# Performance work log

Hardware: AMD Instinct MI355X
Metric: run time of the kernel (lower is better)

## Reference

```python
import jax, jax.numpy as jnp
import numpy as np

N, E, B, D, OUT_D = 10000, 160000, 64, 1024, 128

def setup_inputs() -> dict:
    key = jax.random.key(0)
    ks = jax.random.split(key, 18)
    s = 0.02
    return {
        "pro1_x": jax.random.normal(ks[0], (N, D), jnp.float32),
        "pro1_edge_index": jax.random.randint(ks[1], (2, E), 0, N, jnp.int64 if jax.config.jax_enable_x64 else jnp.int32),
        "pro1_batch": jnp.sort(jax.random.randint(ks[2], (N,), 0, B)),
        "pro2_x": jax.random.normal(ks[3], (N, D), jnp.float32),
        "pro2_edge_index": jax.random.randint(ks[4], (2, E), 0, N, jnp.int64 if jax.config.jax_enable_x64 else jnp.int32),
        "pro2_batch": jnp.sort(jax.random.randint(ks[5], (N,), 0, B)),
        "W1": jax.random.normal(ks[6], (D, D), jnp.float32) * s,
        "b1": jnp.zeros((D,), jnp.float32),
        "fc1_W": jax.random.normal(ks[7], (D, OUT_D), jnp.float32) * s,
        "fc1_b": jnp.zeros((OUT_D,), jnp.float32),
        "W2": jax.random.normal(ks[8], (D, D), jnp.float32) * s,
        "b2": jnp.zeros((D,), jnp.float32),
        "fc2_W": jax.random.normal(ks[9], (D, OUT_D), jnp.float32) * s,
        "fc2_b": jnp.zeros((OUT_D,), jnp.float32),
        "final_W": jax.random.normal(ks[10], (2 * OUT_D, 1), jnp.float32) * s,
        "final_b": jnp.zeros((1,), jnp.float32),
    }

def leaky_relu(x):
    return jnp.where(x >= 0, x, 0.01 * x)

def gcn_conv(x, edge_index, W, b):
    # PyG GCNConv with default add_self_loops + symmetric normalization
    src, dst = edge_index[0], edge_index[1]
    h = x @ W  # [N, D]
    deg = jnp.zeros((x.shape[0],), x.dtype).at[dst].add(1.0) + 1.0  # in-degree + self-loop
    dinv = jax.lax.rsqrt(deg)
    norm = dinv[src] * dinv[dst]  # [E]
    agg = jax.ops.segment_sum(h[src] * norm[:, None], dst, num_segments=x.shape[0])
    agg = agg + h * (1.0 / deg)[:, None]  # self-loop contribution: deg^-1/2 * deg^-1/2
    return agg + b

def global_mean_pool(x, batch, num_graphs):
    sums = jax.ops.segment_sum(x, batch, num_segments=num_graphs)
    cnt = jax.ops.segment_sum(jnp.ones((x.shape[0],), x.dtype), batch, num_segments=num_graphs)
    return sums / jnp.maximum(cnt, 1.0)[:, None]

def reference(pro1_x, pro1_edge_index, pro1_batch, pro2_x, pro2_edge_index, pro2_batch,
              W1, b1, fc1_W, fc1_b, W2, b2, fc2_W, fc2_b, final_W, final_b):
    # branch 1
    x = leaky_relu(gcn_conv(pro1_x, pro1_edge_index, W1, b1))
    x = global_mean_pool(x, pro1_batch, B)
    x = leaky_relu(x @ fc1_W + fc1_b)  # dropout is identity in eval
    # branch 2
    xt = leaky_relu(gcn_conv(pro2_x, pro2_edge_index, W2, b2))
    xt = global_mean_pool(xt, pro2_batch, B)
    xt = leaky_relu(xt @ fc2_W + fc2_b)
    combined = jnp.concatenate([x, xt], axis=1)  # [B, 256]
    return combined @ final_W + final_b
```

## Files before the change

### kernel.cpp

```cpp
#include <hip/hip_runtime.h>
#include <stdint.h>

typedef __attribute__((ext_vector_type(8))) short short8;
typedef __attribute__((ext_vector_type(8))) __bf16 bf16x8;
typedef __attribute__((ext_vector_type(4))) float f32x4;

__device__ inline unsigned short f2bf(float f) {
  unsigned u = __float_as_uint(f);
  unsigned r = (u + 0x7FFFu + ((u >> 16) & 1u)) >> 16;
  return (unsigned short)r;
}
__device__ inline float bflo(unsigned v) { return __uint_as_float(v << 16); }
__device__ inline float bfhi(unsigned v) { return __uint_as_float(v & 0xFFFF0000u); }
__device__ inline bf16x8 as_bf(short8 v) { return __builtin_bit_cast(bf16x8, v); }

#define GLOAD_LDS16(gp, lp)                                                   \
  __builtin_amdgcn_global_load_lds(                                           \
      (const __attribute__((address_space(1))) void*)(gp),                    \
      (__attribute__((address_space(3))) void*)(lp), 16, 0, 0)

#define NG 2048
#define NSL 8

__global__ void prep1_kernel(const float* __restrict__ x0, const float* __restrict__ x1,
                             unsigned short* __restrict__ xb0, unsigned short* __restrict__ xb1,
                             const float* __restrict__ W0, const float* __restrict__ W1,
                             unsigned short* __restrict__ Wt0, unsigned short* __restrict__ Wt1,
                             const int* __restrict__ ei0, const int* __restrict__ ei1,
                             int* __restrict__ dg0, int* __restrict__ dg1,
                             int n, int mpad, int E, int CB) {
  __shared__ float tile[32][33];
  int br = blockIdx.y;
  int b = blockIdx.x;
  int t = threadIdx.x;
  if (b < CB) {
    const float* x = br ? x1 : x0;
    unsigned short* xb = br ? xb1 : xb0;
    long i = (long)b * 256 + t;
    long total = (long)mpad * 128;
    if (i >= total) return;
    long e0 = i * 8;
    int row = (int)(e0 >> 10);
    short8 v;
    if (row < n) {
      const float* s = x + e0;
      float4 fa = *(const float4*)(s);
      float4 fb = *(const float4*)(s + 4);
      v[0] = (short)f2bf(fa.x); v[1] = (short)f2bf(fa.y);
      v[2] = (short)f2bf(fa.z); v[3] = (short)f2bf(fa.w);
      v[4] = (short)f2bf(fb.x); v[5] = (short)f2bf(fb.y);
      v[6] = (short)f2bf(fb.z); v[7] = (short)f2bf(fb.w);
    } else {
      v = (short8)0;
    }
    *(short8*)(xb + e0) = v;
  } else if (b < CB + 1024) {
    const float* W = br ? W1 : W0;
    unsigned short* Wt = br ? Wt1 : Wt0;
    int bb = b - CB;
    int bx = bb & 31;
    int by = bb >> 5;
    int tx = t & 31, ty = t >> 5;
#pragma unroll
    for (int r = 0; r < 4; ++r) {
      int k = by * 32 + ty + r * 8;
      tile[ty + r * 8][tx] = W[(long)k * 1024 + bx * 32 + tx];
    }
    __syncthreads();
#pragma unroll
    for (int r = 0; r < 4; ++r) {
      int nrow = bx * 32 + ty + r * 8;
      int kcol = by * 32 + tx;
      Wt[(long)nrow * 1024 + kcol] = f2bf(tile[tx][ty + r * 8]);
    }
  } else {
    const int* ei = br ? ei1 : ei0;
    int* degi = br ? dg1 : dg0;
    int e = (b - CB - 1024) * 256 + t;
    if (e >= E) return;
    atomicAdd(&degi[ei[E + e]], 1);
  }
}

__global__ __launch_bounds__(1024) void scan2_kernel(
    const int* __restrict__ degA, int* __restrict__ offA, int* __restrict__ curA,
    const int* __restrict__ degB, int* __restrict__ offB, int* __restrict__ curB, int n) {
  const int* deg = blockIdx.x ? degB : degA;
  int* off = blockIdx.x ? offB : offA;
  int* cur = blockIdx.x ? curB : curA;
  __shared__ int wsum[17];
  int t = threadIdx.x, lane = t & 63, w = t >> 6;
  int CH = (n + 1023) >> 10;
  int i0 = t * CH;
  int s = 0;
  for (int i = 0; i < CH; ++i) {
    int idx = i0 + i;
    s += (idx < n) ? ((deg[idx] + 4) & ~3) : 0;
  }
  int inc = s;
  for (int d = 1; d < 64; d <<= 1) {
    int x = __shfl_up(inc, d);
    if (lane >= d) inc += x;
  }
  if (lane == 63) wsum[w] = inc;
  __syncthreads();
  if (t == 0) {
    int r = 0;
    for (int k = 0; k < 16; ++k) { int x = wsum[k]; wsum[k] = r; r += x; }
    wsum[16] = r;
  }
  __syncthreads();
  int run = wsum[w] + inc - s;
  for (int i = 0; i < CH; ++i) {
    int idx = i0 + i;
    if (idx < n) {
      off[idx] = run;
      cur[idx] = run;
      run += (deg[idx] + 4) & ~3;
    }
  }
  if (t == 0) off[n] = wsum[16];
}

__global__ void prep2_kernel(const int* __restrict__ ei0, const int* __restrict__ ei1,
                             const int* __restrict__ dg0, const int* __restrict__ dg1,
                             int* __restrict__ cur0, int* __restrict__ cur1,
                             uint2* __restrict__ cw0, uint2* __restrict__ cw1,
                             const int* __restrict__ off0, const int* __restrict__ off1,
                             int* __restrict__ rng0, int* __restrict__ rng1,
                             int E, int N, int FB) {
  int br = blockIdx.y;
  int b = blockIdx.x;
  int t = threadIdx.x;
  if (b < FB) {
    const int* ei = br ? ei1 : ei0;
    const int* dg = br ? dg1 : dg0;
    int* cur = br ? cur1 : cur0;
    uint2* cw = br ? cw1 : cw0;
    int e = b * 256 + t;
    if (e >= E + N) return;
    int s, d; float w;
    if (e < E) {
      s = ei[e]; d = ei[E + e];
      w = rsqrtf((float)(dg[s] + 1)) * rsqrtf((float)(dg[d] + 1));
    } else {
      s = e - E; d = s;
      w = 1.0f / (float)(dg[s] + 1);
    }
    int p = atomicAdd(&cur[d], 1);
    uint2 v; v.x = (unsigned)s * 2048u; v.y = __float_as_uint(w);
    cw[p] = v;
  } else {
    const int* off = br ? off1 : off0;
    int* rng = br ? rng1 : rng0;
    int q = (b - FB) * 256 + t;
    if (q > NG) return;
    if (q == NG) { rng[q] = N; return; }
    long Etot = off[N];
    long target = (long)q * Etot;
    int lo = 0, hi = N;
    while (lo < hi) {
      int mid = (lo + hi) >> 1;
      if ((long)off[mid] * NG >= target) hi = mid; else lo = mid + 1;
    }
    rng[q] = lo;
  }
}

#define BM 128
#define BN 128
#define BK 64

__global__ __launch_bounds__(256) void gemm_bf16_kernel(
    const unsigned short* __restrict__ A0, const unsigned short* __restrict__ A1,
    const unsigned short* __restrict__ B0, const unsigned short* __restrict__ B1,
    unsigned short* __restrict__ C0, unsigned short* __restrict__ C1,
    int Nn, int K) {
  const unsigned short* A = blockIdx.z ? A1 : A0;
  const unsigned short* Bt = blockIdx.z ? B1 : B0;
  unsigned short* C = blockIdx.z ? C1 : C0;
  __shared__ alignas(16) unsigned short As[BM * BK];
  __shared__ alignas(16) unsigned short Bs[BN * BK];
  int x = blockIdx.x;
  long m0 = (long)((x >> 6) * 8 + (x & 7)) * BM;
  long n0 = (long)((x >> 3) & 7) * BN;
  int t = threadIdx.x;
  int lane = t & 63;
  int w = t >> 6;
  int wm = (w >> 1) * 64, wn = (w & 1) * 64;
  int l3 = lane >> 3;
  int gsw = (lane & 7) ^ l3;
  int srowb = w * 8 + l3;
  const unsigned short* Ag = A + (m0 + srowb) * K + gsw * 8;
  const unsigned short* Bg = Bt + (n0 + srowb) * K + gsw * 8;
  unsigned short* AsP = As + t * 8;
  unsigned short* BsP = Bs + t * 8;
  int fr = lane & 15;
  int c0 = (lane >> 4) ^ (lane & 7);
  const unsigned short* afp0 = As + (wm + fr) * BK + c0 * 8;
  const unsigned short* afp1 = As + (wm + fr) * BK + (c0 ^ 4) * 8;
  const unsigned short* bfp0 = Bs + (wn + fr) * BK + c0 * 8;
  const unsigned short* bfp1 = Bs + (wn + fr) * BK + (c0 ^ 4) * 8;
  f32x4 acc[4][4] = {};
  for (int k0 = 0; k0 < K; k0 += BK) {
    __syncthreads();
#pragma unroll
    for (int j = 0; j < 4; ++j) {
      GLOAD_LDS16(Ag + (long)(j * 32) * K + k0, AsP + j * 2048);
      GLOAD_LDS16(Bg + (long)(j * 32) * K + k0, BsP + j * 2048);
    }
    __syncthreads();
    short8 af[4][2], bf[4][2];
#pragma unroll
    for (int i = 0; i < 4; ++i) {
      af[i][0] = *(const short8*)(afp0 + i * 16 * BK);
      af[i][1] = *(const short8*)(afp1 + i * 16 * BK);
    }
#pragma unroll
    for (int i = 0; i < 4; ++i) {
      bf[i][0] = *(const short8*)(bfp0 + i * 16 * BK);
      bf[i][1] = *(const short8*)(bfp1 + i * 16 * BK);
    }
#pragma unroll
    for (int i = 0; i < 4; ++i)
#pragma unroll
      for (int j = 0; j < 4; ++j) {
        acc[i][j] = __builtin_amdgcn_mfma_f32_16x16x32_bf16(as_bf(af[i][0]), as_bf(bf[j][0]),
                                                            acc[i][j], 0, 0, 0);
        acc[i][j] = __builtin_amdgcn_mfma_f32_16x16x32_bf16(as_bf(af[i][1]), as_bf(bf[j][1]),
                                                            acc[i][j], 0, 0, 0);
      }
  }
  int cr = (lane >> 4) * 4;
  int cc = lane & 15;
#pragma unroll
  for (int i = 0; i < 4; ++i)
#pragma unroll
    for (int j = 0; j < 4; ++j) {
      long row = m0 + wm + i * 16 + cr;
      long col = n0 + wn + j * 16 + cc;
      unsigned short* cp = C + row * Nn + col;
#pragma unroll
      for (int r = 0; r < 4; ++r)
        cp[(long)r * Nn] = f2bf(acc[i][j][r]);
    }
}

__global__ __launch_bounds__(256) void agg_pool_kernel(
    const unsigned short* __restrict__ H0, const unsigned short* __restrict__ H1,
    const int* __restrict__ off0, const int* __restrict__ off1,
    const uint2* __restrict__ cw0, const uint2* __restrict__ cw1,
    const int* __restrict__ b0, const int* __restrict__ b1,
    const int* __restrict__ rng0, const int* __restrict__ rng1,
    const float* __restrict__ bias0, const float* __restrict__ bias1,
    float* __restrict__ pool0, float* __restrict__ pool1,
    float* __restrict__ scr0, float* __restrict__ scr1,
    int* __restrict__ gid0, int* __restrict__ gid1) {
  int br = blockIdx.y;
  const uint8_t* Hb = (const uint8_t*)(br ? H1 : H0);
  const int* off = br ? off1 : off0;
  const uint2* cw = br ? cw1 : cw0;
  const int* batch = br ? b1 : b0;
  const int* rng = br ? rng1 : rng0;
  const float* bias = br ? bias1 : bias0;
  float* pool = br ? pool1 : pool0;
  float* scratch = br ? scr1 : scr0;
  int* gid = br ? gid1 : gid0;

  int t = threadIdx.x;
  int wv = t >> 6, lane = t & 63, qw = lane >> 4, l16 = lane & 15;
  int slice = blockIdx.x & 7;
  int part = blockIdx.x >> 3;
  int q = part * 4 + wv;
  int d0 = slice * 128 + l16 * 8;
  unsigned d0b = (unsigned)d0 * 2;
  int na = rng[q], nb = rng[q + 1];
  int g0 = -1, g1 = -1;
  if (na < nb) {
    float4 bv0 = *(const float4*)(bias + d0);
    float4 bv1 = *(const float4*)(bias + d0 + 4);
    float bv[8] = {bv0.x, bv0.y, bv0.z, bv0.w, bv1.x, bv1.y, bv1.z, bv1.w};
    float pacc[8] = {};
    float a[8] = {};
    int curg = batch[na];
    int fi = 0;
    int nd = na;
    int ee = off[na + 1];
    int eend = off[nb];
    int e = off[na];
    uint2 cc = cw[e + qw];
    uint2 cn = cw[e + 4 + qw];
    uint4 hc = *(const uint4*)(Hb + (cc.x + d0b));
#pragma unroll 2
    for (; e < eend; e += 4) {
      uint4 hn = *(const uint4*)(Hb + (cn.x + d0b));
      uint2 c2 = cw[e + 8 + qw];
      float w = __uint_as_float(cc.y);
      a[0] += w * bflo(hc.x); a[1] += w * bfhi(hc.x);
      a[2] += w * bflo(hc.y); a[3] += w * bfhi(hc.y);
      a[4] += w * bflo(hc.z); a[5] += w * bfhi(hc.z);
      a[6] += w * bflo(hc.w); a[7] += w * bfhi(hc.w);
      cc = cn; cn = c2; hc = hn;
      if (e + 4 == ee) {
#pragma unroll
        for (int k = 0; k < 8; ++k) {
          float v = a[k];
          v += __shfl_xor(v, 16);
          v += __shfl_xor(v, 32);
          v += bv[k];
          pacc[k] += (v >= 0.f) ? v : 0.01f * v;
          a[k] = 0.f;
        }
        ++nd;
        if (nd < nb) {
          ee = off[nd + 1];
          int g = batch[nd];
          if (g != curg) {
            if (fi == 0) {
              g0 = curg;
              if (qw == 0) {
                float* sp = scratch + ((long)q * 2 + 0) * 1024 + d0;
                *(float4*)sp = make_float4(pacc[0], pacc[1], pacc[2], pacc[3]);
                *(float4*)(sp + 4) = make_float4(pacc[4], pacc[5], pacc[6], pacc[7]);
              }
            } else {
              if (qw == 0) {
                float* pp = pool + (long)curg * 1024 + d0;
#pragma unroll
                for (int k = 0; k < 8; ++k) atomicAdd(pp + k, pacc[k]);
              }
            }
            ++fi;
#pragma unroll
            for (int k = 0; k < 8; ++k) pacc[k] = 0.f;
            curg = g;
          }
        }
      }
    }
    if (fi == 0) {
      g0 = curg;
      if (qw == 0) {
        float* sp = scratch + ((long)q * 2 + 0) * 1024 + d0;
        *(float4*)sp = make_float4(pacc[0], pacc[1], pacc[2], pacc[3]);
        *(float4*)(sp + 4) = make_float4(pacc[4], pacc[5], pacc[6], pacc[7]);
      }
    } else {
      g1 = curg;
      if (qw == 0) {
        float* sp = scratch + ((long)q * 2 + 1) * 1024 + d0;
        *(float4*)sp = make_float4(pacc[0], pacc[1], pacc[2], pacc[3]);
        *(float4*)(sp + 4) = make_float4(pacc[4], pacc[5], pacc[6], pacc[7]);
      }
    }
  }
  if (slice == 0 && lane == 0) {
    gid[q * 2] = g0;
    gid[q * 2 + 1] = g1;
  }
}

__global__ __launch_bounds__(256) void pool_reduce_kernel(
    const float* __restrict__ scr0, const float* __restrict__ scr1,
    const int* __restrict__ gid0, const int* __restrict__ gid1,
    const int* __restrict__ b0, const int* __restrict__ b1,
    const int* __restrict__ rng0, const int* __restrict__ rng1,
    float* __restrict__ pool0, float* __restrict__ pool1, int N) {
  int br = blockIdx.y;
  const float* scratch = br ? scr1 : scr0;
  const int* gid = br ? gid1 : gid0;
  const int* batch = br ? b1 : b0;
  const int* rng = br ? rng1 : rng0;
  float* pool = br ? pool1 : pool0;
  int g = blockIdx.x >> 2;
  int slice = blockIdx.x & 3;
  int tid = threadIdx.x;
  int lo = 0, hi = N;
  while (lo < hi) { int m = (lo + hi) >> 1; if (batch[m] < g) lo = m + 1; else hi = m; }
  int gs = lo;
  lo = 0; hi = N;
  while (lo < hi) { int m = (lo + hi) >> 1; if (batch[m] <= g) lo = m + 1; else hi = m; }
  int ge = lo;
  if (gs >= ge) return;
  lo = 0; hi = NG - 1;
  while (lo < hi) { int m = (lo + hi) >> 1; if (rng[m + 1] > gs) hi = m; else lo = m + 1; }
  int qlo = lo;
  lo = 0; hi = NG - 1;
  while (lo < hi) { int m = (lo + hi + 1) >> 1; if (rng[m] < ge) lo = m; else hi = m - 1; }
  int qhi = lo;
  float s = 0.f;
  for (int q = qlo; q <= qhi; ++q) {
    int a = gid[q * 2], b = gid[q * 2 + 1];
    if (a == g) s += scratch[((long)q * 2 + 0) * 1024 + slice * 256 + tid];
    if (b == g) s += scratch[((long)q * 2 + 1) * 1024 + slice * 256 + tid];
  }
  long idx = (long)g * 1024 + slice * 256 + tid;
  pool[idx] += s;
}

__global__ __launch_bounds__(256) void fc_final_kernel(
    const float* __restrict__ pool1, const float* __restrict__ pool2,
    const int* __restrict__ b0, const int* __restrict__ b1, int N,
    const float* __restrict__ fc1W, const float* __restrict__ fc1b,
    const float* __restrict__ fc2W, const float* __restrict__ fc2b,
    const float* __restrict__ finW, const float* __restrict__ finb,
    float* __restrict__ out) {
  __shared__ float p1[1024], p2[1024];
  __shared__ float red[256];
  int g = blockIdx.x, t = threadIdx.x;
  int lo = 0, hi = N;
  while (lo < hi) { int m = (lo + hi) >> 1; if (b0[m] < g) lo = m + 1; else hi = m; }
  int gs = lo;
  lo = 0; hi = N;
  while (lo < hi) { int m = (lo + hi) >> 1; if (b0[m] <= g) lo = m + 1; else hi = m; }
  float ic1 = 1.0f / (float)max(lo - gs, 1);
  lo = 0; hi = N;
  while (lo < hi) { int m = (lo + hi) >> 1; if (b1[m] < g) lo = m + 1; else hi = m; }
  gs = lo;
  lo = 0; hi = N;
  while (lo < hi) { int m = (lo + hi) >> 1; if (b1[m] <= g) lo = m + 1; else hi = m; }
  float ic2 = 1.0f / (float)max(lo - gs, 1);
  for (int i = t; i < 1024; i += 256) {
    p1[i] = pool1[(long)g * 1024 + i] * ic1;
    p2[i] = pool2[(long)g * 1024 + i] * ic2;
  }
  __syncthreads();
  float contrib;
  if (t < 128) {
    float a = 0.f;
    for (int k = 0; k < 1024; ++k) a += p1[k] * fc1W[(long)k * 128 + t];
    a += fc1b[t];
    a = a >= 0.f ? a : 0.01f * a;
    contrib = a * finW[t];
  } else {
    int j = t - 128;
    float a = 0.f;
    for (int k = 0; k < 1024; ++k) a += p2[k] * fc2W[(long)k * 128 + j];
    a += fc2b[j];
    a = a >= 0.f ? a : 0.01f * a;
    contrib = a * finW[128 + j];
  }
  red[t] = contrib;
  __syncthreads();
  for (int s = 128; s; s >>= 1) {
    if (t < s) red[t] += red[t + s];
    __syncthreads();
  }
  if (t == 0) out[g] = red[0] + finb[0];
}

extern "C" void kernel_launch(void* const* d_in, const int* in_sizes, int n_in,
                              void* d_out, int out_size, void* d_ws, size_t ws_size,
                              hipStream_t stream) {
  (void)n_in; (void)ws_size;
  const float* xs[2]   = {(const float*)d_in[0], (const float*)d_in[3]};
  const int* eis[2]    = {(const int*)d_in[1], (const int*)d_in[4]};
  const int* bts[2]    = {(const int*)d_in[2], (const int*)d_in[5]};
  const float* Ws[2]   = {(const float*)d_in[6], (const float*)d_in[10]};
  const float* bs[2]   = {(const float*)d_in[7], (const float*)d_in[11]};
  const float* fc1W = (const float*)d_in[8];
  const float* fc1b = (const float*)d_in[9];
  const float* fc2W = (const float*)d_in[12];
  const float* fc2b = (const float*)d_in[13];
  const float* finW = (const float*)d_in[14];
  const float* finb = (const float*)d_in[15];
  float* out = (float*)d_out;

  const int N = in_sizes[2];
  const int E = in_sizes[1] / 2;
  const int Mpad = ((N + 1023) / 1024) * 1024;
  const int MT = Mpad / BM;
  const int CWCAP = E + 4 * N + 64;

  uint8_t* ws = (uint8_t*)d_ws;
  size_t o = 0;
  auto alloc = [&](size_t bytes) { size_t r = o; o += (bytes + 255) & ~(size_t)255; return r; };
  size_t degi_o[2] = {alloc((size_t)N * 4), alloc((size_t)N * 4)};
  size_t pool_o[2] = {alloc((size_t)out_size * 1024 * 4), alloc((size_t)out_size * 1024 * 4)};
  size_t cw_o[2]   = {alloc((size_t)CWCAP * 8), alloc((size_t)CWCAP * 8)};
  size_t zero_end = o;
  size_t cur_o[2]  = {alloc((size_t)N * 4), alloc((size_t)N * 4)};
  size_t off_o[2]  = {alloc((size_t)(N + 1) * 4), alloc((size_t)(N + 1) * 4)};
  size_t rng_o[2]  = {alloc((size_t)(NG + 1) * 4), alloc((size_t)(NG + 1) * 4)};
  size_t gid_o[2]  = {alloc((size_t)NG * 2 * 4), alloc((size_t)NG * 2 * 4)};
  size_t scr_o[2]  = {alloc((size_t)NG * 2 * 1024 * 4), alloc((size_t)NG * 2 * 1024 * 4)};
  size_t xb_o[2]   = {alloc((size_t)Mpad * 1024 * 2), alloc((size_t)Mpad * 1024 * 2)};
  size_t wt_o[2]   = {alloc((size_t)1024 * 1024 * 2), alloc((size_t)1024 * 1024 * 2)};
  size_t h_o[2]    = {alloc((size_t)Mpad * 1024 * 2), alloc((size_t)Mpad * 1024 * 2)};

  (void)hipMemsetAsync(ws, 0, zero_end, stream);

  const int CB = (int)(((long)Mpad * 128 + 255) / 256);
  const int DB = (E + 255) / 256;
  prep1_kernel<<<dim3(CB + 1024 + DB, 2), 256, 0, stream>>>(
      xs[0], xs[1], (unsigned short*)(ws + xb_o[0]), (unsigned short*)(ws + xb_o[1]),
      Ws[0], Ws[1], (unsigned short*)(ws + wt_o[0]), (unsigned short*)(ws + wt_o[1]),
      eis[0], eis[1], (int*)(ws + degi_o[0]), (int*)(ws + degi_o[1]),
      N, Mpad, E, CB);
  scan2_kernel<<<2, 1024, 0, stream>>>(
      (const int*)(ws + degi_o[0]), (int*)(ws + off_o[0]), (int*)(ws + cur_o[0]),
      (const int*)(ws + degi_o[1]), (int*)(ws + off_o[1]), (int*)(ws + cur_o[1]), N);
  const int FB = (E + N + 255) / 256;
  const int RB = (NG + 256) / 256;
  prep2_kernel<<<dim3(FB + RB, 2), 256, 0, stream>>>(
      eis[0], eis[1], (const int*)(ws + degi_o[0]), (const int*)(ws + degi_o[1]),
      (int*)(ws + cur_o[0]), (int*)(ws + cur_o[1]),
      (uint2*)(ws + cw_o[0]), (uint2*)(ws + cw_o[1]),
      (const int*)(ws + off_o[0]), (const int*)(ws + off_o[1]),
      (int*)(ws + rng_o[0]), (int*)(ws + rng_o[1]), E, N, FB);
  gemm_bf16_kernel<<<dim3(MT * 8, 1, 2), 256, 0, stream>>>(
      (const unsigned short*)(ws + xb_o[0]), (const unsigned short*)(ws + xb_o[1]),
      (const unsigned short*)(ws + wt_o[0]), (const unsigned short*)(ws + wt_o[1]),
      (unsigned short*)(ws + h_o[0]), (unsigned short*)(ws + h_o[1]), 1024, 1024);
  agg_pool_kernel<<<dim3((NG / 4) * NSL, 2), 256, 0, stream>>>(
      (const unsigned short*)(ws + h_o[0]), (const unsigned short*)(ws + h_o[1]),
      (const int*)(ws + off_o[0]), (const int*)(ws + off_o[1]),
      (const uint2*)(ws + cw_o[0]), (const uint2*)(ws + cw_o[1]),
      bts[0], bts[1],
      (const int*)(ws + rng_o[0]), (const int*)(ws + rng_o[1]),
      bs[0], bs[1],
      (float*)(ws + pool_o[0]), (float*)(ws + pool_o[1]),
      (float*)(ws + scr_o[0]), (float*)(ws + scr_o[1]),
      (int*)(ws + gid_o[0]), (int*)(ws + gid_o[1]));
  pool_reduce_kernel<<<dim3(out_size * 4, 2), 256, 0, stream>>>(
      (const float*)(ws + scr_o[0]), (const float*)(ws + scr_o[1]),
      (const int*)(ws + gid_o[0]), (const int*)(ws + gid_o[1]),
      bts[0], bts[1],
      (const int*)(ws + rng_o[0]), (const int*)(ws + rng_o[1]),
      (float*)(ws + pool_o[0]), (float*)(ws + pool_o[1]), N);
  fc_final_kernel<<<out_size, 256, 0, stream>>>(
      (const float*)(ws + pool_o[0]), (const float*)(ws + pool_o[1]),
      bts[0], bts[1], N,
      fc1W, fc1b, fc2W, fc2b, finW, finb, out);
}
```

Measured before the change: 237.3 us.

## Fuse fp32-to-bf16 conversion into GEMM loads and merge pool reduce into fc

Measured after the change: 270.8 us. +14.1%, slower.

```diff
diff --git a/kernel.cpp b/kernel.cpp
--- a/kernel.cpp
+++ b/kernel.cpp
@@ -4,6 +4,7 @@
 typedef __attribute__((ext_vector_type(8))) short short8;
 typedef __attribute__((ext_vector_type(8))) __bf16 bf16x8;
 typedef __attribute__((ext_vector_type(4))) float f32x4;
+typedef __attribute__((ext_vector_type(2))) float f32x2;
 
 __device__ inline unsigned short f2bf(float f) {
   unsigned u = __float_as_uint(f);
@@ -13,53 +14,39 @@
 __device__ inline float bflo(unsigned v) { return __uint_as_float(v << 16); }
 __device__ inline float bfhi(unsigned v) { return __uint_as_float(v & 0xFFFF0000u); }
 __device__ inline bf16x8 as_bf(short8 v) { return __builtin_bit_cast(bf16x8, v); }
+__device__ inline f32x2 up2(unsigned u) { f32x2 r; r.x = bflo(u); r.y = bfhi(u); return r; }
+__device__ inline unsigned cvtpk(float lo, float hi) {
+  unsigned r;
+  asm("v_cvt_pk_bf16_f32 %0, %1, %2" : "=v"(r) : "v"(lo), "v"(hi));
+  return r;
+}
+__device__ inline int lbound(const int* a, int n, int v) {
+  int lo = 0, hi = n;
+  while (lo < hi) { int m = (lo + hi) >> 1; if (a[m] < v) lo = m + 1; else hi = m; }
+  return lo;
+}
 
 #define GLOAD_LDS16(gp, lp)                                                   \
   __builtin_amdgcn_global_load_lds(                                           \
       (const __attribute__((address_space(1))) void*)(gp),                    \
       (__attribute__((address_space(3))) void*)(lp), 16, 0, 0)
 
-#define NG 2048
+#define NG 1024
 #define NSL 8
 
-__global__ void prep1_kernel(const float* __restrict__ x0, const float* __restrict__ x1,
-                             unsigned short* __restrict__ xb0, unsigned short* __restrict__ xb1,
-                             const float* __restrict__ W0, const float* __restrict__ W1,
+__global__ void prep1_kernel(const float* __restrict__ W0, const float* __restrict__ W1,
                              unsigned short* __restrict__ Wt0, unsigned short* __restrict__ Wt1,
                              const int* __restrict__ ei0, const int* __restrict__ ei1,
-                             int* __restrict__ dg0, int* __restrict__ dg1,
-                             int n, int mpad, int E, int CB) {
+                             int* __restrict__ dg0, int* __restrict__ dg1, int E) {
   __shared__ float tile[32][33];
   int br = blockIdx.y;
   int b = blockIdx.x;
   int t = threadIdx.x;
-  if (b < CB) {
-    const float* x = br ? x1 : x0;
-    unsigned short* xb = br ? xb1 : xb0;
-    long i = (long)b * 256 + t;
-    long total = (long)mpad * 128;
-    if (i >= total) return;
-    long e0 = i * 8;
-    int row = (int)(e0 >> 10);
-    short8 v;
-    if (row < n) {
-      const float* s = x + e0;
-      float4 fa = *(const float4*)(s);
-      float4 fb = *(const float4*)(s + 4);
-      v[0] = (short)f2bf(fa.x); v[1] = (short)f2bf(fa.y);
-      v[2] = (short)f2bf(fa.z); v[3] = (short)f2bf(fa.w);
-      v[4] = (short)f2bf(fb.x); v[5] = (short)f2bf(fb.y);
-      v[6] = (short)f2bf(fb.z); v[7] = (short)f2bf(fb.w);
-    } else {
-      v = (short8)0;
-    }
-    *(short8*)(xb + e0) = v;
-  } else if (b < CB + 1024) {
+  if (b < 1024) {
     const float* W = br ? W1 : W0;
     unsigned short* Wt = br ? Wt1 : Wt0;
-    int bb = b - CB;
-    int bx = bb & 31;
-    int by = bb >> 5;
+    int bx = b & 31;
+    int by = b >> 5;
     int tx = t & 31, ty = t >> 5;
 #pragma unroll
     for (int r = 0; r < 4; ++r) {
@@ -76,7 +63,7 @@
   } else {
     const int* ei = br ? ei1 : ei0;
     int* degi = br ? dg1 : dg0;
-    int e = (b - CB - 1024) * 256 + t;
+    int e = (b - 1024) * 256 + t;
     if (e >= E) return;
     atomicAdd(&degi[ei[E + e]], 1);
   }
@@ -172,11 +159,11 @@
 #define BK 64
 
 __global__ __launch_bounds__(256) void gemm_bf16_kernel(
-    const unsigned short* __restrict__ A0, const unsigned short* __restrict__ A1,
+    const float* __restrict__ X0, const float* __restrict__ X1,
     const unsigned short* __restrict__ B0, const unsigned short* __restrict__ B1,
     unsigned short* __restrict__ C0, unsigned short* __restrict__ C1,
-    int Nn, int K) {
-  const unsigned short* A = blockIdx.z ? A1 : A0;
+    int Nrows, int Nn, int K) {
+  const float* X = blockIdx.z ? X1 : X0;
   const unsigned short* Bt = blockIdx.z ? B1 : B0;
   unsigned short* C = blockIdx.z ? C1 : C0;
   __shared__ alignas(16) unsigned short As[BM * BK];
@@ -191,10 +178,20 @@
   int l3 = lane >> 3;
   int gsw = (lane & 7) ^ l3;
   int srowb = w * 8 + l3;
-  const unsigned short* Ag = A + (m0 + srowb) * K + gsw * 8;
   const unsigned short* Bg = Bt + (n0 + srowb) * K + gsw * 8;
-  unsigned short* AsP = As + t * 8;
   unsigned short* BsP = Bs + t * 8;
+  const float* Asrc[4];
+  unsigned short* AsW[4];
+  bool okA[4];
+#pragma unroll
+  for (int j = 0; j < 4; ++j) {
+    int c = j * 256 + t;
+    int row = c >> 3;
+    int cc8 = c & 7;
+    Asrc[j] = X + (m0 + row) * (long)K + cc8 * 8;
+    AsW[j] = As + row * BK + (cc8 ^ (row & 7)) * 8;
+    okA[j] = (m0 + row) < Nrows;
+  }
   int fr = lane & 15;
   int c0 = (lane >> 4) ^ (lane & 7);
   const unsigned short* afp0 = As + (wm + fr) * BK + c0 * 8;
@@ -205,9 +202,21 @@
   for (int k0 = 0; k0 < K; k0 += BK) {
     __syncthreads();
 #pragma unroll
+    for (int j = 0; j < 4; ++j)
+      GLOAD_LDS16(Bg + (long)(j * 32) * K + k0, BsP + j * 2048);
+#pragma unroll
     for (int j = 0; j < 4; ++j) {
-      GLOAD_LDS16(Ag + (long)(j * 32) * K + k0, AsP + j * 2048);
-      GLOAD_LDS16(Bg + (long)(j * 32) * K + k0, BsP + j * 2048);
+      float4 f0 = make_float4(0.f, 0.f, 0.f, 0.f), f1 = f0;
+      if (okA[j]) {
+        f0 = *(const float4*)(Asrc[j] + k0);
+        f1 = *(const float4*)(Asrc[j] + k0 + 4);
+      }
+      uint4 pk;
+      pk.x = cvtpk(f0.x, f0.y);
+      pk.y = cvtpk(f0.z, f0.w);
+      pk.z = cvtpk(f1.x, f1.y);
+      pk.w = cvtpk(f1.z, f1.w);
+      *(uint4*)AsW[j] = pk;
     }
     __syncthreads();
     short8 af[4][2], bf[4][2];
@@ -274,14 +283,14 @@
   int q = part * 4 + wv;
   int d0 = slice * 128 + l16 * 8;
   unsigned d0b = (unsigned)d0 * 2;
+  float4 bv0 = *(const float4*)(bias + d0);
+  float4 bv1 = *(const float4*)(bias + d0 + 4);
   int na = rng[q], nb = rng[q + 1];
   int g0 = -1, g1 = -1;
   if (na < nb) {
-    float4 bv0 = *(const float4*)(bias + d0);
-    float4 bv1 = *(const float4*)(bias + d0 + 4);
     float bv[8] = {bv0.x, bv0.y, bv0.z, bv0.w, bv1.x, bv1.y, bv1.z, bv1.w};
     float pacc[8] = {};
-    float a[8] = {};
+    f32x2 a2[4] = {};
     int curg = batch[na];
     int fi = 0;
     int nd = na;
@@ -296,21 +305,23 @@
       uint4 hn = *(const uint4*)(Hb + (cn.x + d0b));
       uint2 c2 = cw[e + 8 + qw];
       float w = __uint_as_float(cc.y);
-      a[0] += w * bflo(hc.x); a[1] += w * bfhi(hc.x);
-      a[2] += w * bflo(hc.y); a[3] += w * bfhi(hc.y);
-      a[4] += w * bflo(hc.z); a[5] += w * bfhi(hc.z);
-      a[6] += w * bflo(hc.w); a[7] += w * bfhi(hc.w);
+      f32x2 w2; w2.x = w; w2.y = w;
+      a2[0] += w2 * up2(hc.x);
+      a2[1] += w2 * up2(hc.y);
+      a2[2] += w2 * up2(hc.z);
+      a2[3] += w2 * up2(hc.w);
       cc = cn; cn = c2; hc = hn;
       if (e + 4 == ee) {
 #pragma unroll
         for (int k = 0; k < 8; ++k) {
-          float v = a[k];
+          float v = (k & 1) ? a2[k >> 1].y : a2[k >> 1].x;
           v += __shfl_xor(v, 16);
           v += __shfl_xor(v, 32);
           v += bv[k];
           pacc[k] += (v >= 0.f) ? v : 0.01f * v;
-          a[k] = 0.f;
         }
+#pragma unroll
+        for (int k = 0; k < 4; ++k) { a2[k].x = 0.f; a2[k].y = 0.f; }
         ++nd;
         if (nd < nb) {
           ee = off[nd + 1];
@@ -360,46 +371,11 @@
   }
 }
 
-__global__ __launch_bounds__(256) void pool_reduce_kernel(
+__global__ __launch_bounds__(256) void fc_final_kernel(
+    const float* __restrict__ pool1, const float* __restrict__ pool2,
     const float* __restrict__ scr0, const float* __restrict__ scr1,
     const int* __restrict__ gid0, const int* __restrict__ gid1,
-    const int* __restrict__ b0, const int* __restrict__ b1,
     const int* __restrict__ rng0, const int* __restrict__ rng1,
-    float* __restrict__ pool0, float* __restrict__ pool1, int N) {
-  int br = blockIdx.y;
-  const float* scratch = br ? scr1 : scr0;
-  const int* gid = br ? gid1 : gid0;
-  const int* batch = br ? b1 : b0;
-  const int* rng = br ? rng1 : rng0;
-  float* pool = br ? pool1 : pool0;
-  int g = blockIdx.x >> 2;
-  int slice = blockIdx.x & 3;
-  int tid = threadIdx.x;
-  int lo = 0, hi = N;
-  while (lo < hi) { int m = (lo + hi) >> 1; if (batch[m] < g) lo = m + 1; else hi = m; }
-  int gs = lo;
-  lo = 0; hi = N;
-  while (lo < hi) { int m = (lo + hi) >> 1; if (batch[m] <= g) lo = m + 1; else hi = m; }
-  int ge = lo;
-  if (gs >= ge) return;
-  lo = 0; hi = NG - 1;
-  while (lo < hi) { int m = (lo + hi) >> 1; if (rng[m + 1] > gs) hi = m; else lo = m + 1; }
-  int qlo = lo;
-  lo = 0; hi = NG - 1;
-  while (lo < hi) { int m = (lo + hi + 1) >> 1; if (rng[m] < ge) lo = m; else hi = m - 1; }
-  int qhi = lo;
-  float s = 0.f;
-  for (int q = qlo; q <= qhi; ++q) {
-    int a = gid[q * 2], b = gid[q * 2 + 1];
-    if (a == g) s += scratch[((long)q * 2 + 0) * 1024 + slice * 256 + tid];
-    if (b == g) s += scratch[((long)q * 2 + 1) * 1024 + slice * 256 + tid];
-  }
-  long idx = (long)g * 1024 + slice * 256 + tid;
-  pool[idx] += s;
-}
-
-__global__ __launch_bounds__(256) void fc_final_kernel(
-    const float* __restrict__ pool1, const float* __restrict__ pool2,
     const int* __restrict__ b0, const int* __restrict__ b1, int N,
     const float* __restrict__ fc1W, const float* __restrict__ fc1b,
     const float* __restrict__ fc2W, const float* __restrict__ fc2b,
@@ -408,21 +384,27 @@
   __shared__ float p1[1024], p2[1024];
   __shared__ float red[256];
   int g = blockIdx.x, t = threadIdx.x;
-  int lo = 0, hi = N;
-  while (lo < hi) { int m = (lo + hi) >> 1; if (b0[m] < g) lo = m + 1; else hi = m; }
-  int gs = lo;
-  lo = 0; hi = N;
-  while (lo < hi) { int m = (lo + hi) >> 1; if (b0[m] <= g) lo = m + 1; else hi = m; }
-  float ic1 = 1.0f / (float)max(lo - gs, 1);
-  lo = 0; hi = N;
-  while (lo < hi) { int m = (lo + hi) >> 1; if (b1[m] < g) lo = m + 1; else hi = m; }
-  gs = lo;
-  lo = 0; hi = N;
-  while (lo < hi) { int m = (lo + hi) >> 1; if (b1[m] <= g) lo = m + 1; else hi = m; }
-  float ic2 = 1.0f / (float)max(lo - gs, 1);
+  int gs0 = lbound(b0, N, g), ge0 = lbound(b0, N, g + 1);
+  float ic1 = 1.0f / (float)max(ge0 - gs0, 1);
+  int qlo0 = max(lbound(rng0, NG + 1, gs0 + 1) - 1, 0);
+  int qhi0 = min(lbound(rng0, NG + 1, ge0) - 1, NG - 1);
+  int gs1 = lbound(b1, N, g), ge1 = lbound(b1, N, g + 1);
+  float ic2 = 1.0f / (float)max(ge1 - gs1, 1);
+  int qlo1 = max(lbound(rng1, NG + 1, gs1 + 1) - 1, 0);
+  int qhi1 = min(lbound(rng1, NG + 1, ge1) - 1, NG - 1);
   for (int i = t; i < 1024; i += 256) {
-    p1[i] = pool1[(long)g * 1024 + i] * ic1;
-    p2[i] = pool2[(long)g * 1024 + i] * ic2;
+    float s1 = pool1[(long)g * 1024 + i];
+    for (int q = qlo0; q <= qhi0; ++q) {
+      if (gid0[q * 2] == g)     s1 += scr0[((long)q * 2 + 0) * 1024 + i];
+      if (gid0[q * 2 + 1] == g) s1 += scr0[((long)q * 2 + 1) * 1024 + i];
+    }
+    p1[i] = s1 * ic1;
+    float s2 = pool2[(long)g * 1024 + i];
+    for (int q = qlo1; q <= qhi1; ++q) {
+      if (gid1[q * 2] == g)     s2 += scr1[((long)q * 2 + 0) * 1024 + i];
+      if (gid1[q * 2 + 1] == g) s2 += scr1[((long)q * 2 + 1) * 1024 + i];
+    }
+    p2[i] = s2 * ic2;
   }
   __syncthreads();
   float contrib;
@@ -484,19 +466,15 @@
   size_t rng_o[2]  = {alloc((size_t)(NG + 1) * 4), alloc((size_t)(NG + 1) * 4)};
   size_t gid_o[2]  = {alloc((size_t)NG * 2 * 4), alloc((size_t)NG * 2 * 4)};
   size_t scr_o[2]  = {alloc((size_t)NG * 2 * 1024 * 4), alloc((size_t)NG * 2 * 1024 * 4)};
-  size_t xb_o[2]   = {alloc((size_t)Mpad * 1024 * 2), alloc((size_t)Mpad * 1024 * 2)};
   size_t wt_o[2]   = {alloc((size_t)1024 * 1024 * 2), alloc((size_t)1024 * 1024 * 2)};
   size_t h_o[2]    = {alloc((size_t)Mpad * 1024 * 2), alloc((size_t)Mpad * 1024 * 2)};
 
   (void)hipMemsetAsync(ws, 0, zero_end, stream);
 
-  const int CB = (int)(((long)Mpad * 128 + 255) / 256);
   const int DB = (E + 255) / 256;
-  prep1_kernel<<<dim3(CB + 1024 + DB, 2), 256, 0, stream>>>(
-      xs[0], xs[1], (unsigned short*)(ws + xb_o[0]), (unsigned short*)(ws + xb_o[1]),
+  prep1_kernel<<<dim3(1024 + DB, 2), 256, 0, stream>>>(
       Ws[0], Ws[1], (unsigned short*)(ws + wt_o[0]), (unsigned short*)(ws + wt_o[1]),
-      eis[0], eis[1], (int*)(ws + degi_o[0]), (int*)(ws + degi_o[1]),
-      N, Mpad, E, CB);
+      eis[0], eis[1], (int*)(ws + degi_o[0]), (int*)(ws + degi_o[1]), E);
   scan2_kernel<<<2, 1024, 0, stream>>>(
       (const int*)(ws + degi_o[0]), (int*)(ws + off_o[0]), (int*)(ws + cur_o[0]),
       (const int*)(ws + degi_o[1]), (int*)(ws + off_o[1]), (int*)(ws + cur_o[1]), N);
@@ -509,9 +487,9 @@
       (const int*)(ws + off_o[0]), (const int*)(ws + off_o[1]),
       (int*)(ws + rng_o[0]), (int*)(ws + rng_o[1]), E, N, FB);
   gemm_bf16_kernel<<<dim3(MT * 8, 1, 2), 256, 0, stream>>>(
-      (const unsigned short*)(ws + xb_o[0]), (const unsigned short*)(ws + xb_o[1]),
+      xs[0], xs[1],
       (const unsigned short*)(ws + wt_o[0]), (const unsigned short*)(ws + wt_o[1]),
-      (unsigned short*)(ws + h_o[0]), (unsigned short*)(ws + h_o[1]), 1024, 1024);
+      (unsigned short*)(ws + h_o[0]), (unsigned short*)(ws + h_o[1]), N, 1024, 1024);
   agg_pool_kernel<<<dim3((NG / 4) * NSL, 2), 256, 0, stream>>>(
       (const unsigned short*)(ws + h_o[0]), (const unsigned short*)(ws + h_o[1]),
       (const int*)(ws + off_o[0]), (const int*)(ws + off_o[1]),
@@ -522,14 +500,11 @@
       (float*)(ws + pool_o[0]), (float*)(ws + pool_o[1]),
       (float*)(ws + scr_o[0]), (float*)(ws + scr_o[1]),
       (int*)(ws + gid_o[0]), (int*)(ws + gid_o[1]));
-  pool_reduce_kernel<<<dim3(out_size * 4, 2), 256, 0, stream>>>(
+  fc_final_kernel<<<out_size, 256, 0, stream>>>(
+      (const float*)(ws + pool_o[0]), (const float*)(ws + pool_o[1]),
       (const float*)(ws + scr_o[0]), (const float*)(ws + scr_o[1]),
       (const int*)(ws + gid_o[0]), (const int*)(ws + gid_o[1]),
-      bts[0], bts[1],
       (const int*)(ws + rng_o[0]), (const int*)(ws + rng_o[1]),
-      (float*)(ws + pool_o[0]), (float*)(ws + pool_o[1]), N);
-  fc_final_kernel<<<out_size, 256, 0, stream>>>(
-      (const float*)(ws + pool_o[0]), (const float*)(ws + pool_o[1]),
       bts[0], bts[1], N,
       fc1W, fc1b, fc2W, fc2b, finW, finb, out);
 }
```
